# Kernel optimization log

Measured on AMD Instinct MI355X. Metric: run time of the kernel, lower is better.

The kernel has to match this reference:

```python
import math
import jax, jax.numpy as jnp
import numpy as np

B, T, C, H = 4, 1024, 1024, 16


def setup_inputs() -> dict:
    key = jax.random.key(0)
    k1, k2, k3 = jax.random.split(key, 3)
    scale = 0.02
    return {
        "x": jax.random.normal(k1, (B, T, C), dtype=jnp.float32),
        "w_attn": jax.random.normal(k2, (C, 3 * C), dtype=jnp.float32) * scale,
        "b_attn": jnp.zeros((3 * C,), dtype=jnp.float32),
        "w_proj": jax.random.normal(k3, (C, C), dtype=jnp.float32) * scale,
        "b_proj": jnp.zeros((C,), dtype=jnp.float32),
    }


def reference(x, w_attn, b_attn, w_proj, b_proj):
    b, t, c = x.shape
    h = H
    d = c // h
    qkv = x @ w_attn + b_attn                      # [b, t, 3c]
    q, k, v = jnp.split(qkv, 3, axis=-1)
    # [b, h, t, d]
    q = q.reshape(b, t, h, d).transpose(0, 2, 1, 3)
    k = k.reshape(b, t, h, d).transpose(0, 2, 1, 3)
    v = v.reshape(b, t, h, d).transpose(0, 2, 1, 3)
    att = jnp.einsum("bhqd,bhkd->bhqk", q, k) * (1.0 / math.sqrt(d))
    causal = jnp.tril(jnp.ones((t, t), dtype=bool))
    att = jnp.where(causal[None, None], att, -jnp.inf)
    att = jax.nn.softmax(att, axis=-1)
    # dropout is identity in eval mode
    y = jnp.einsum("bhqk,bhkd->bhqd", att, v)      # [b, h, t, d]
    y = y.transpose(0, 2, 1, 3).reshape(b, t, c)
    return y @ w_proj + b_proj
```

## Files before the change

### kernel.cpp

```cpp
#include <hip/hip_runtime.h>

typedef __bf16 bf16;
typedef float f32x4 __attribute__((ext_vector_type(4)));
typedef bf16 bf16x4 __attribute__((ext_vector_type(4)));
typedef bf16 bf16x8 __attribute__((ext_vector_type(8)));

#define MFMA16(a, b, c) __builtin_amdgcn_mfma_f32_16x16x32_bf16((a), (b), (c), 0, 0, 0)

__device__ __forceinline__ f32x4 zero4() {
    f32x4 z; z[0] = 0.f; z[1] = 0.f; z[2] = 0.f; z[3] = 0.f; return z;
}
__device__ __forceinline__ float max3f(float a, float b, float c) {
    return fmaxf(fmaxf(a, b), c);
}
__device__ __forceinline__ void gl_lds16(const bf16* g, bf16* l) {
    __builtin_amdgcn_global_load_lds(
        (const __attribute__((address_space(1))) void*)g,
        (__attribute__((address_space(3))) void*)l, 16, 0, 0);
}

__global__ __launch_bounds__(256)
void prep_k(const float* __restrict__ x, bf16* __restrict__ xb,
            const float* __restrict__ w_attn, bf16* __restrict__ wT,
            const float* __restrict__ w_proj, bf16* __restrict__ wpT)
{
    __shared__ bf16 Ls[64][72];
    const int blk = blockIdx.x;
    const int tid = threadIdx.x;

    if (blk < 2048) {
        const int i = (blk * 256 + tid) * 8;
        const float4 a = *(const float4*)(x + i);
        const float4 b = *(const float4*)(x + i + 4);
        bf16x8 o;
        o[0] = (bf16)a.x; o[1] = (bf16)a.y; o[2] = (bf16)a.z; o[3] = (bf16)a.w;
        o[4] = (bf16)b.x; o[5] = (bf16)b.y; o[6] = (bf16)b.z; o[7] = (bf16)b.w;
        *(bf16x8*)(xb + i) = o;
        return;
    }
    const float* src;
    bf16* dst;
    int K, N, bx, by;
    if (blk < 2816) {
        const int r = blk - 2048;
        src = w_attn; dst = wT; K = 1024; N = 3072;
        bx = r % 48; by = r / 48;
    } else {
        const int r = blk - 2816;
        src = w_proj; dst = wpT; K = 1024; N = 1024;
        bx = r & 15; by = r >> 4;
    }
    const int k0 = by << 6;
    const int n0 = bx << 6;
    #pragma unroll
    for (int it = 0; it < 4; ++it) {
        const int lin = (it << 10) + (tid << 2);
        const int r = lin >> 6, c = lin & 63;
        const float4 v = *(const float4*)(src + (size_t)(k0 + r) * N + n0 + c);
        bf16x4 o; o[0] = (bf16)v.x; o[1] = (bf16)v.y; o[2] = (bf16)v.z; o[3] = (bf16)v.w;
        *(bf16x4*)&Ls[r][c] = o;
    }
    __syncthreads();
    #pragma unroll
    for (int it = 0; it < 2; ++it) {
        const int lin = (it << 11) + (tid << 3);
        const int nn = lin >> 6, kk = lin & 63;
        bf16x8 o;
        #pragma unroll
        for (int j = 0; j < 8; ++j) o[j] = Ls[kk + j][nn];
        *(bf16x8*)(dst + (size_t)(n0 + nn) * K + k0 + kk) = o;
    }
}

template <int MODE>
__global__ __launch_bounds__(256)
void gemm_bt(const bf16* __restrict__ A, const bf16* __restrict__ Bt,
             const float* __restrict__ bias,
             bf16* __restrict__ qw, bf16* __restrict__ kw, bf16* __restrict__ vw,
             float* __restrict__ outf)
{
    constexpr int BK = 32;
    constexpr int BN = (MODE == 0) ? 128 : 64;
    constexpr int K  = 1024;
    constexpr int N  = (MODE == 0) ? 3072 : 1024;
    constexpr int MF = (MODE == 0) ? 4 : 2;
    constexpr int NF = 4;
    constexpr int AE = 128 * BK;
    constexpr int BE = BN * BK;
    constexpr int nk = K / BK;

    __shared__ __align__(16) bf16 smem[3 * (AE + BE)];
    bf16* const Asb = smem;
    bf16* const Bsb = smem + 3 * AE;

    const int tid  = threadIdx.x;
    const int lane = tid & 63;
    const int wid  = tid >> 6;
    const int l16  = lane & 15;
    const int g    = lane >> 4;
    const int wrb  = (MODE == 0) ? ((wid >> 1) << 6) : (wid << 5);
    const int wcb  = (MODE == 0) ? ((wid & 1) << 6) : 0;

    const int p   = blockIdx.x;
    const int xcd = p & 7;
    const int r   = p >> 3;
    int by, bx;
    if (MODE == 0) { by = ((xcd >> 1) << 3) + r / 12; bx = (xcd & 1) * 12 + r % 12; }
    else           { by = ((xcd >> 1) << 3) + (r >> 3); bx = ((xcd & 1) << 3) + (r & 7); }
    const int m0 = by << 7;
    const int n0 = bx * BN;

    const int srow = lane >> 2;
    const int schk = lane & 3;
    const int rA0 = (wid << 5) + srow;
    const int rA1 = rA0 + 16;
    const int rB0 = wid * (BN / 4) + srow;
    const int rB1 = rB0 + 16;
    const bf16* const pa0 = A  + (size_t)(m0 + rA0) * K + ((schk ^ ((rA0 >> 1) & 3)) << 3);
    const bf16* const pa1 = A  + (size_t)(m0 + rA1) * K + ((schk ^ ((rA1 >> 1) & 3)) << 3);
    const bf16* const pb0 = Bt + (size_t)(n0 + rB0) * K + ((schk ^ ((rB0 >> 1) & 3)) << 3);
    const bf16* const pb1 = Bt + (size_t)(n0 + rB1) * K + ((schk ^ ((rB1 >> 1) & 3)) << 3);
    const int dA0 = (wid << 5) * BK, dA1 = dA0 + 16 * BK;
    const int dB0 = (wid * (BN / 4)) * BK, dB1 = dB0 + 16 * BK;

    int offA[MF], offB[NF];
    #pragma unroll
    for (int mf = 0; mf < MF; ++mf) {
        const int rr = wrb + (mf << 4) + l16;
        offA[mf] = rr * BK + ((g ^ ((rr >> 1) & 3)) << 3);
    }
    #pragma unroll
    for (int nf = 0; nf < NF; ++nf) {
        const int rr = wcb + (nf << 4) + l16;
        offB[nf] = rr * BK + ((g ^ ((rr >> 1) & 3)) << 3);
    }

    f32x4 acc[MF][NF];
    #pragma unroll
    for (int i = 0; i < MF; ++i)
        #pragma unroll
        for (int j = 0; j < NF; ++j) acc[i][j] = zero4();

    auto issue = [&](int t, int s) {
        bf16* const ab = Asb + s * AE;
        bf16* const bb = Bsb + s * BE;
        gl_lds16(pa0 + t * BK, ab + dA0);
        gl_lds16(pa1 + t * BK, ab + dA1);
        gl_lds16(pb0 + t * BK, bb + dB0);
        if constexpr (MODE == 0) gl_lds16(pb1 + t * BK, bb + dB1);
    };

    issue(0, 0);
    issue(1, 1);

    #pragma unroll
    for (int kt = 0; kt < nk; ++kt) {
        if (kt == nk - 1) {
            asm volatile("s_waitcnt vmcnt(0)" ::: "memory");
        } else {
            if constexpr (MODE == 0) asm volatile("s_waitcnt vmcnt(4)" ::: "memory");
            else                     asm volatile("s_waitcnt vmcnt(3)" ::: "memory");
        }
        __builtin_amdgcn_s_barrier();
        if (kt + 2 < nk) issue(kt + 2, (kt + 2) % 3);
        const bf16* const ac = Asb + (kt % 3) * AE;
        const bf16* const bc = Bsb + (kt % 3) * BE;
        bf16x8 af[MF], bfr[NF];
        #pragma unroll
        for (int mf = 0; mf < MF; ++mf) af[mf] = *(const bf16x8*)&ac[offA[mf]];
        #pragma unroll
        for (int nf = 0; nf < NF; ++nf) bfr[nf] = *(const bf16x8*)&bc[offB[nf]];
        __builtin_amdgcn_s_setprio(1);
        #pragma unroll
        for (int mf = 0; mf < MF; ++mf)
            #pragma unroll
            for (int nf = 0; nf < NF; ++nf)
                acc[mf][nf] = MFMA16(af[mf], bfr[nf], acc[mf][nf]);
        __builtin_amdgcn_s_setprio(0);
    }
    __syncthreads();

    if (MODE == 0) {
        bf16* const Es = smem;
        const int bq  = m0 >> 10;
        const int tb  = m0 & 1023;
        const int hh0 = (n0 & 1023) >> 6;
        const bool isV = (n0 >= 2048);
        if (isV) {
            #pragma unroll
            for (int mf = 0; mf < MF; ++mf)
                #pragma unroll
                for (int nf = 0; nf < NF; ++nf) {
                    const int nn = wcb + (nf << 4) + l16;
                    const float bs = bias[n0 + nn];
                    bf16x4 pq;
                    #pragma unroll
                    for (int j = 0; j < 4; ++j) pq[j] = (bf16)(acc[mf][nf][j] + bs);
                    const int m = wrb + (mf << 4) + (g << 2);
                    const int pp = ((m >> 5) << 5) + (((m >> 2) & 3) << 3) + (((m >> 4) & 1) << 2);
                    *(bf16x4*)&Es[nn * 128 + pp] = pq;
                }
        } else {
            #pragma unroll
            for (int mf = 0; mf < MF; ++mf)
                #pragma unroll
                for (int nf = 0; nf < NF; ++nf) {
                    const int nn = wcb + (nf << 4) + l16;
                    const float bs = bias[n0 + nn];
                    #pragma unroll
                    for (int j = 0; j < 4; ++j) {
                        const int mm = wrb + (mf << 4) + (g << 2) + j;
                        Es[mm * 128 + nn] = (bf16)(acc[mf][nf][j] + bs);
                    }
                }
        }
        __syncthreads();
        #pragma unroll
        for (int it = 0; it < 8; ++it) {
            const int idx = (it << 8) + tid;
            const int row = idx >> 4, ch = idx & 15;
            const bf16x8 v = *(const bf16x8*)&Es[row * 128 + (ch << 3)];
            if (isV) {
                const int dd = row & 63, hh = hh0 + (row >> 6);
                *(bf16x8*)(vw + ((size_t)((bq << 4) + hh) << 16) + ((size_t)dd << 10)
                           + tb + (ch << 3)) = v;
            } else {
                const int t = tb + row;
                const int cc = ch << 3;
                const int hh = hh0 + (cc >> 6);
                bf16* const dst = (n0 < 1024) ? qw : kw;
                *(bf16x8*)(dst + ((size_t)((bq << 4) + hh) << 16) + ((size_t)t << 6)
                           + (cc & 63)) = v;
            }
        }
    } else {
        #pragma unroll
        for (int mf = 0; mf < MF; ++mf)
            #pragma unroll
            for (int nf = 0; nf < NF; ++nf) {
                const int ng = n0 + wcb + (nf << 4) + l16;
                const float bs = bias[ng];
                #pragma unroll
                for (int j = 0; j < 4; ++j) {
                    const int mg = m0 + wrb + (mf << 4) + (g << 2) + j;
                    outf[(size_t)mg * N + ng] = acc[mf][nf][j] + bs;
                }
            }
    }
}

__global__ __launch_bounds__(256)
void attn_k(const bf16* __restrict__ Qp, const bf16* __restrict__ Kp,
            const bf16* __restrict__ Vt, bf16* __restrict__ att)
{
    __shared__ __align__(16) bf16 Kl0[4096], Kl1[4096];
    __shared__ __align__(16) bf16 Vl0[4096], Vl1[4096];

    const int p   = blockIdx.x;
    const int xcd = p & 7;
    const int i   = p >> 3;
    const int bh  = (xcd << 3) + (i & 7);
    const int iq  = i >> 3;
    const int a   = iq >> 2, qs = iq & 3;
    const int qb  = (a == 0) ? (15 - qs) : (a == 1) ? (8 + qs)
                  : (a == 2) ? (7 - qs) : qs;
    const int b   = bh >> 4, h = bh & 15;

    const int tid  = threadIdx.x;
    const int lane = tid & 63;
    const int wid  = tid >> 6;
    const int g    = lane >> 4;
    const int l16  = lane & 15;
    const int g8   = g << 3;

    const size_t hb = (size_t)bh << 16;
    const bf16* Qh = Qp + hb;
    const bf16* Kh = Kp + hb;
    const bf16* Vh = Vt + hb;

    const int srow = lane >> 3;
    const int sswz = ((lane & 7) ^ srow) << 3;
    const int kr0  = (wid << 4) + srow;
    const int kr1  = kr0 + 8;
    const int dst0 = (wid << 4) << 6;
    const int dst1 = ((wid << 4) + 8) << 6;

    int offKV[2][4];
    #pragma unroll
    for (int ks = 0; ks < 2; ++ks)
        #pragma unroll
        for (int cb = 0; cb < 4; ++cb) {
            const int r = (cb << 4) + l16;
            offKV[ks][cb] = (r << 6) + (((((ks << 2) + g)) ^ (r & 7)) << 3);
        }

    const float QSCALE = 0.125f * 1.44269504f;
    const int qloc = (wid << 4) + l16;
    const int q0 = qb << 6;

    const bf16* qp = Qh + ((size_t)(q0 + qloc) << 6) + g8;
    bf16x8 qf0 = *(const bf16x8*)qp, qf1 = *(const bf16x8*)(qp + 32);
    #pragma unroll
    for (int e = 0; e < 8; ++e) {
        qf0[e] = (bf16)(QSCALE * (float)qf0[e]);
        qf1[e] = (bf16)(QSCALE * (float)qf1[e]);
    }

    f32x4 acc_o[4];
    float m_r = -1e30f, l_r = 0.f;
    #pragma unroll
    for (int i2 = 0; i2 < 4; ++i2) acc_o[i2] = zero4();

    auto stage = [&](int t, bf16* Kn, bf16* Vn) {
        const int kv = t << 6;
        gl_lds16(Kh + ((size_t)(kv + kr0) << 6) + sswz, Kn + dst0);
        gl_lds16(Kh + ((size_t)(kv + kr1) << 6) + sswz, Kn + dst1);
        gl_lds16(Vh + ((size_t)kr0 << 10) + kv + sswz, Vn + dst0);
        gl_lds16(Vh + ((size_t)kr1 << 10) + kv + sswz, Vn + dst1);
    };

    stage(0, Kl0, Vl0);

    for (int kt = 0; kt <= qb; ++kt) {
        const bool odd = kt & 1;
        if (kt < qb) {
            stage(kt + 1, odd ? Kl0 : Kl1, odd ? Vl0 : Vl1);
            asm volatile("s_waitcnt vmcnt(4)" ::: "memory");
        } else {
            asm volatile("s_waitcnt vmcnt(0)" ::: "memory");
        }
        __builtin_amdgcn_s_barrier();
        const bf16* Kc = odd ? Kl1 : Kl0;
        const bf16* Vc = odd ? Vl1 : Vl0;

        bf16x8 kf[2][4], vf[2][4];
        #pragma unroll
        for (int ks = 0; ks < 2; ++ks)
            #pragma unroll
            for (int cb = 0; cb < 4; ++cb) {
                kf[ks][cb] = *(const bf16x8*)&Kc[offKV[ks][cb]];
                vf[ks][cb] = *(const bf16x8*)&Vc[offKV[ks][cb]];
            }

        f32x4 sacc[4];
        #pragma unroll
        for (int cb = 0; cb < 4; ++cb) sacc[cb] = zero4();
        #pragma unroll
        for (int cb = 0; cb < 4; ++cb) sacc[cb] = MFMA16(kf[0][cb], qf0, sacc[cb]);
        #pragma unroll
        for (int cb = 0; cb < 4; ++cb) sacc[cb] = MFMA16(kf[1][cb], qf1, sacc[cb]);
        if (kt == qb) {
            #pragma unroll
            for (int cb = 0; cb < 4; ++cb)
                #pragma unroll
                for (int j = 0; j < 4; ++j)
                    if (((cb << 4) + (g << 2) + j) > qloc) sacc[cb][j] = -1e30f;
        }
        const float t0 = max3f(sacc[0][0], sacc[0][1], sacc[0][2]);
        const float t1 = max3f(sacc[0][3], sacc[1][0], sacc[1][1]);
        const float t2 = max3f(sacc[1][2], sacc[1][3], sacc[2][0]);
        const float t3 = max3f(sacc[2][1], sacc[2][2], sacc[2][3]);
        const float t4 = max3f(sacc[3][0], sacc[3][1], sacc[3][2]);
        float pm = fmaxf(max3f(t0, t1, t2), max3f(t3, t4, sacc[3][3]));
        pm = fmaxf(pm, __shfl_xor(pm, 16));
        pm = fmaxf(pm, __shfl_xor(pm, 32));
        if (__any(pm > m_r + 8.f)) {
            const float mn = fmaxf(m_r, pm);
            const float sc = __builtin_amdgcn_exp2f(m_r - mn);
            m_r = mn; l_r *= sc;
            #pragma unroll
            for (int db = 0; db < 4; ++db)
                #pragma unroll
                for (int j = 0; j < 4; ++j) acc_o[db][j] *= sc;
        }
        float rsum = 0.f;
        #pragma unroll
        for (int cb = 0; cb < 4; ++cb)
            #pragma unroll
            for (int j = 0; j < 4; ++j) {
                const float pv = __builtin_amdgcn_exp2f(sacc[cb][j] - m_r);
                sacc[cb][j] = pv;
                rsum += pv;
            }
        rsum += __shfl_xor(rsum, 16);
        rsum += __shfl_xor(rsum, 32);
        l_r += rsum;
        bf16x8 pf0, pf1;
        #pragma unroll
        for (int e = 0; e < 8; ++e) {
            pf0[e] = (bf16)sacc[e >> 2][e & 3];
            pf1[e] = (bf16)sacc[2 + (e >> 2)][e & 3];
        }
        #pragma unroll
        for (int db = 0; db < 4; ++db) acc_o[db] = MFMA16(vf[0][db], pf0, acc_o[db]);
        #pragma unroll
        for (int db = 0; db < 4; ++db) acc_o[db] = MFMA16(vf[1][db], pf1, acc_o[db]);

        asm volatile("" ::: "memory");
        __builtin_amdgcn_s_barrier();
        asm volatile("" ::: "memory");
    }

    const float inv = 1.f / l_r;
    const int t = q0 + qloc;
    #pragma unroll
    for (int db = 0; db < 4; ++db) {
        bf16x4 o;
        #pragma unroll
        for (int j = 0; j < 4; ++j) o[j] = (bf16)(acc_o[db][j] * inv);
        *(bf16x4*)(att + (((size_t)b << 10) + t) * 1024 + (h << 6) + (db << 4) + (g << 2)) = o;
    }
}

extern "C" void kernel_launch(void* const* d_in, const int* in_sizes, int n_in,
                              void* d_out, int out_size, void* d_ws, size_t ws_size,
                              hipStream_t stream)
{
    const float* x      = (const float*)d_in[0];
    const float* w_attn = (const float*)d_in[1];
    const float* b_attn = (const float*)d_in[2];
    const float* w_proj = (const float*)d_in[3];
    const float* b_proj = (const float*)d_in[4];
    float* out = (float*)d_out;

    bf16* xb  = (bf16*)d_ws;
    bf16* wT  = xb  + (size_t)4096 * 1024;
    bf16* wpT = wT  + (size_t)3072 * 1024;
    bf16* qw  = wpT + (size_t)1024 * 1024;
    bf16* kw  = qw  + (size_t)64 * 1024 * 64;
    bf16* vw  = kw  + (size_t)64 * 1024 * 64;
    bf16* aw  = vw  + (size_t)64 * 1024 * 64;

    prep_k<<<3072, 256, 0, stream>>>(x, xb, w_attn, wT, w_proj, wpT);

    gemm_bt<0><<<768, 256, 0, stream>>>(xb, wT, b_attn, qw, kw, vw, nullptr);
    attn_k<<<1024, 256, 0, stream>>>(qw, kw, vw, aw);
    gemm_bt<1><<<512, 256, 0, stream>>>(aw, wpT, b_proj, nullptr, nullptr, nullptr, out);
}
```

Measured before the change: 81.96 us.

## Triple-buffer K/V tiles in attention, drop trailing barrier, add MFMA priority hints

Result: slower. 84.79 us (+3.4%).

```diff
diff --git a/kernel.cpp b/kernel.cpp
--- a/kernel.cpp
+++ b/kernel.cpp
@@ -253,8 +253,8 @@
 void attn_k(const bf16* __restrict__ Qp, const bf16* __restrict__ Kp,
             const bf16* __restrict__ Vt, bf16* __restrict__ att)
 {
-    __shared__ __align__(16) bf16 Kl0[4096], Kl1[4096];
-    __shared__ __align__(16) bf16 Vl0[4096], Vl1[4096];
+    __shared__ __align__(16) bf16 Kls[3 * 4096];
+    __shared__ __align__(16) bf16 Vls[3 * 4096];
 
     const int p   = blockIdx.x;
     const int xcd = p & 7;
@@ -311,27 +311,28 @@
     #pragma unroll
     for (int i2 = 0; i2 < 4; ++i2) acc_o[i2] = zero4();
 
-    auto stage = [&](int t, bf16* Kn, bf16* Vn) {
+    auto stage = [&](int t, int s) {
         const int kv = t << 6;
+        bf16* const Kn = Kls + s * 4096;
+        bf16* const Vn = Vls + s * 4096;
         gl_lds16(Kh + ((size_t)(kv + kr0) << 6) + sswz, Kn + dst0);
         gl_lds16(Kh + ((size_t)(kv + kr1) << 6) + sswz, Kn + dst1);
         gl_lds16(Vh + ((size_t)kr0 << 10) + kv + sswz, Vn + dst0);
         gl_lds16(Vh + ((size_t)kr1 << 10) + kv + sswz, Vn + dst1);
     };
 
-    stage(0, Kl0, Vl0);
+    stage(0, 0);
+    if (qb >= 1) stage(1, 1);
 
     for (int kt = 0; kt <= qb; ++kt) {
-        const bool odd = kt & 1;
-        if (kt < qb) {
-            stage(kt + 1, odd ? Kl0 : Kl1, odd ? Vl0 : Vl1);
-            asm volatile("s_waitcnt vmcnt(4)" ::: "memory");
-        } else {
-            asm volatile("s_waitcnt vmcnt(0)" ::: "memory");
-        }
+        const int slot = kt % 3;
+        if (kt < qb) asm volatile("s_waitcnt vmcnt(4)" ::: "memory");
+        else         asm volatile("s_waitcnt vmcnt(0)" ::: "memory");
         __builtin_amdgcn_s_barrier();
-        const bf16* Kc = odd ? Kl1 : Kl0;
-        const bf16* Vc = odd ? Vl1 : Vl0;
+        if (kt + 2 <= qb) stage(kt + 2, (kt + 2) % 3);
+
+        const bf16* Kc = Kls + slot * 4096;
+        const bf16* Vc = Vls + slot * 4096;
 
         bf16x8 kf[2][4], vf[2][4];
         #pragma unroll
@@ -345,10 +346,12 @@
         f32x4 sacc[4];
         #pragma unroll
         for (int cb = 0; cb < 4; ++cb) sacc[cb] = zero4();
+        __builtin_amdgcn_s_setprio(1);
         #pragma unroll
         for (int cb = 0; cb < 4; ++cb) sacc[cb] = MFMA16(kf[0][cb], qf0, sacc[cb]);
         #pragma unroll
         for (int cb = 0; cb < 4; ++cb) sacc[cb] = MFMA16(kf[1][cb], qf1, sacc[cb]);
+        __builtin_amdgcn_s_setprio(0);
         if (kt == qb) {
             #pragma unroll
             for (int cb = 0; cb < 4; ++cb)
@@ -391,14 +394,12 @@
             pf0[e] = (bf16)sacc[e >> 2][e & 3];
             pf1[e] = (bf16)sacc[2 + (e >> 2)][e & 3];
         }
+        __builtin_amdgcn_s_setprio(1);
         #pragma unroll
         for (int db = 0; db < 4; ++db) acc_o[db] = MFMA16(vf[0][db], pf0, acc_o[db]);
         #pragma unroll
         for (int db = 0; db < 4; ++db) acc_o[db] = MFMA16(vf[1][db], pf1, acc_o[db]);
-
-        asm volatile("" ::: "memory");
-        __builtin_amdgcn_s_barrier();
-        asm volatile("" ::: "memory");
+        __builtin_amdgcn_s_setprio(0);
     }
 
     const float inv = 1.f / l_r;
```
